# Kernel optimization log

Hardware: AMD Instinct MI355X
Metric: run time of the kernel (lower is better)

The kernel has to match this reference:

```python
import jax, jax.numpy as jnp
from jax import lax
import numpy as np

B, L, FEAT, EXTRA, K1 = 128, 128, 36, 12, 3
EMB, H, A, T_OUT = 6, 1024, 256, 24
CONV_OUT = FEAT - 2 * (K1 - 1)  # 32


def _conv1d(x, w):
    return lax.conv_general_dilated(x, w, (1,), 'VALID', dimension_numbers=('NCW', 'OIW', 'NCW'))


def _lstm(x_t, h, c, Wih, Whh, b):
    g = x_t @ Wih.T + h @ Whh.T + b
    i, f, gg, o = jnp.split(g, 4, axis=-1)
    c = jax.nn.sigmoid(f) * c + jax.nn.sigmoid(i) * jnp.tanh(gg)
    h = jax.nn.sigmoid(o) * jnp.tanh(c)
    return h, c


def setup_inputs():
    key = jax.random.key(0)
    ks = jax.random.split(key, 20)
    s = 0.05
    r = lambda k, sh: jax.random.normal(k, sh, jnp.float32) * s
    return {
        'x': jax.random.normal(ks[0], (B, L, FEAT + EXTRA), jnp.float32),
        'conv1_w': r(ks[1], (L, L, K1)), 'conv1_b': r(ks[2], (L,)),
        'conv2_w': r(ks[3], (L, L, K1)), 'conv2_b': r(ks[4], (L,)),
        'lin3_w': r(ks[5], (EMB, CONV_OUT)), 'lin3_b': r(ks[6], (EMB,)),
        'enc_Wih': r(ks[7], (4 * H, EMB + EXTRA)), 'enc_Whh': r(ks[8], (4 * H, H)), 'enc_b': r(ks[9], (4 * H,)),
        'attn_Wq': r(ks[10], (A, H)), 'attn_Wk': r(ks[11], (A, H)), 'attn_Wv': r(ks[12], (1, A)),
        'dec_Wih': r(ks[13], (4 * H, 2 * H)), 'dec_Whh': r(ks[14], (4 * H, H)), 'dec_b': r(ks[15], (4 * H,)),
        'out_w': r(ks[16], (1, H)), 'out_b': r(ks[17], (1,)),
    }


def reference(x, conv1_w, conv1_b, conv2_w, conv2_b, lin3_w, lin3_b,
              enc_Wih, enc_Whh, enc_b, attn_Wq, attn_Wk, attn_Wv,
              dec_Wih, dec_Whh, dec_b, out_w, out_b):
    # CNN feature extractor over the dense (short-interval) features
    dense = x[:, :, :FEAT]                                   # (B, L, 36)
    h1 = jax.nn.softplus(_conv1d(dense, conv1_w) + conv1_b[None, :, None])
    h2 = jax.nn.relu(_conv1d(h1, conv2_w) + conv2_b[None, :, None])  # (B, L, 32)
    lin = jnp.einsum('blf,ef->ble', h2, lin3_w) + lin3_b     # (B, L, EMB)
    lstm_in = jnp.concatenate([lin, x[:, :, FEAT:]], axis=2)  # (B, L, EMB+EXTRA)

    # LSTM encoder
    def enc_step(carry, xt):
        h, c = carry
        h, c = _lstm(xt, h, c, enc_Wih, enc_Whh, enc_b)
        return (h, c), h
    z = jnp.zeros((B, H), jnp.float32)
    (h, c), outs = lax.scan(enc_step, (z, z), lstm_in.transpose(1, 0, 2))
    enc_out = outs.transpose(1, 0, 2)                        # (B, L, H)
    s = enc_out[:, -1]

    # fixed-size key buffer; original appends s_t each step (lengths 128..151)
    M = L - 1 + T_OUT
    buf0 = jnp.zeros((B, M, H), jnp.float32).at[:, :L - 1].set(enc_out[:, :-1])
    pos = jnp.arange(M)

    def dec_step(carry, t):
        h, c, s, buf = carry
        buf = lax.dynamic_update_slice(buf, s[:, None, :], (0, L - 1 + t, 0))
        mask = (pos <= L - 1 + t).astype(buf.dtype)
        q = jnp.stack([h, c], axis=1)                        # (B, 2, H)
        qp = q @ attn_Wq.T                                   # (B, 2, A)
        kp = buf @ attn_Wk.T                                 # (B, M, A)
        feats = jnp.tanh(qp[:, :, None, :] + kp[:, None, :, :])  # (B, 2, M, A)
        scores = jnp.einsum('bnma,a->bnm', feats, attn_Wv[0])
        # original: softmax over dim=1 (query axis); mask keys post-softmax
        w = jax.nn.softmax(scores, axis=1) * mask[None, None, :]
        ctx = jnp.einsum('bnm,bmh->bnh', w, buf).reshape(B, 2 * H)
        h, c = _lstm(ctx, h, c, dec_Wih, dec_Whh, dec_b)
        y = (h @ out_w.T + out_b)[:, 0]
        return (h, c, h, buf), y

    _, ys = lax.scan(dec_step, (h, c, s, buf0), jnp.arange(T_OUT))
    return ys.T                                              # (B, T_OUT)
```

## Files before the change

### kernel.cpp

```cpp
#include <hip/hip_runtime.h>
#include <math.h>


#define NB 128
#define NL 128
#define NH 1024
#define NA 256
#define NT 24
#define NM 151

typedef __attribute__((ext_vector_type(8))) short bf16x8;
typedef __attribute__((ext_vector_type(8))) short s16x8;
typedef __attribute__((ext_vector_type(4))) float f32x4;

#define MFMA(a, b, acc) __builtin_amdgcn_mfma_f32_16x16x32_bf16(a, b, acc, 0, 0, 0)

#define I16_SCALE 32767.0f
#define I16_INV   (1.0f / 32767.0f)

__device__ __forceinline__ float sig_f(float x) {
  return 1.0f / (1.0f + __expf(-x));
}
__device__ __forceinline__ float tanh_f(float x) {
  x = fminf(9.0f, fmaxf(-9.0f, x));
  float e = __expf(2.0f * x);
  return (e - 1.0f) / (e + 1.0f);
}
__device__ __forceinline__ unsigned short f2bf(float f) {
  unsigned int u = __float_as_uint(f);
  u = (u + 0x7FFFu + ((u >> 16) & 1u)) >> 16;
  return (unsigned short)u;
}
__device__ __forceinline__ float bf2f(unsigned short u) {
  return __uint_as_float(((unsigned int)u) << 16);
}
__device__ __forceinline__ short f2i16(float f) {
  return (short)__float2int_rn(f * I16_SCALE);
}

__global__ __launch_bounds__(128) void conv_front(
    const float* __restrict__ x,
    const float* __restrict__ w1, const float* __restrict__ b1,
    const float* __restrict__ w2, const float* __restrict__ b2,
    const float* __restrict__ w3, const float* __restrict__ b3,
    float* __restrict__ lstm_in)
{
  int b = blockIdx.x;
  int t = threadIdx.x;
  __shared__ float d[128][36];
  __shared__ float h1[128][34];
  __shared__ float h2[128][32];

  const float* xr = x + (size_t)(b * NL + t) * 48;
  #pragma unroll
  for (int f = 0; f < 36; ++f) d[t][f] = xr[f];
  __syncthreads();

  float acc[34];
  {
    float bias = b1[t];
    #pragma unroll
    for (int w = 0; w < 34; ++w) acc[w] = bias;
  }
  const float* wr = w1 + t * 384;
  for (int ci = 0; ci < 128; ++ci) {
    float row[36];
    #pragma unroll
    for (int f = 0; f < 36; ++f) row[f] = d[ci][f];
    float wa = wr[ci * 3 + 0], wb = wr[ci * 3 + 1], wc = wr[ci * 3 + 2];
    #pragma unroll
    for (int w = 0; w < 34; ++w)
      acc[w] += row[w] * wa + row[w + 1] * wb + row[w + 2] * wc;
  }
  #pragma unroll
  for (int w = 0; w < 34; ++w) {
    float z = acc[w];
    h1[t][w] = (z > 20.0f) ? z : log1pf(__expf(z));
  }
  __syncthreads();

  float acc2[32];
  {
    float bias = b2[t];
    #pragma unroll
    for (int w = 0; w < 32; ++w) acc2[w] = bias;
  }
  const float* wr2 = w2 + t * 384;
  for (int ci = 0; ci < 128; ++ci) {
    float row[34];
    #pragma unroll
    for (int f = 0; f < 34; ++f) row[f] = h1[ci][f];
    float wa = wr2[ci * 3 + 0], wb = wr2[ci * 3 + 1], wc = wr2[ci * 3 + 2];
    #pragma unroll
    for (int w = 0; w < 32; ++w)
      acc2[w] += row[w] * wa + row[w + 1] * wb + row[w + 2] * wc;
  }
  #pragma unroll
  for (int w = 0; w < 32; ++w) h2[t][w] = fmaxf(acc2[w], 0.0f);
  __syncthreads();

  float* outr = lstm_in + (size_t)(b * NL + t) * 18;
  #pragma unroll
  for (int e = 0; e < 6; ++e) {
    float s = b3[e];
    #pragma unroll
    for (int f = 0; f < 32; ++f) s += h2[t][f] * w3[e * 32 + f];
    outr[e] = s;
  }
  #pragma unroll
  for (int j = 0; j < 12; ++j) outr[6 + j] = xr[36 + j];
}

__global__ void frag_w(const float* __restrict__ src, int K, int kshift,
                       unsigned short* __restrict__ hi,
                       unsigned short* __restrict__ lo, int ngroups)
{
  int o = blockIdx.x * 256 + threadIdx.x;
  if (o >= ngroups) return;
  int lane = o & 63;
  int ki = (o >> 6) & ((1 << kshift) - 1);
  int tile = (o >> (6 + kshift)) & 1;
  int bx = o >> (7 + kshift);
  int l15 = lane & 15, q = lane >> 4;
  int idx = tile * 16 + l15;
  int grow = (idx >> 3) * 1024 + bx * 8 + (idx & 7);
  const float* s = src + (size_t)grow * K + ki * 32 + q * 8;
  unsigned short hv[8], lv[8];
  #pragma unroll
  for (int j = 0; j < 8; ++j) {
    float v = s[j];
    hv[j] = f2bf(v);
    lv[j] = f2bf(v - bf2f(hv[j]));
  }
  size_t e = (size_t)o * 8;
  *(ushort4*)(hi + e) = make_ushort4(hv[0], hv[1], hv[2], hv[3]);
  *(ushort4*)(hi + e + 4) = make_ushort4(hv[4], hv[5], hv[6], hv[7]);
  *(ushort4*)(lo + e) = make_ushort4(lv[0], lv[1], lv[2], lv[3]);
  *(ushort4*)(lo + e + 4) = make_ushort4(lv[4], lv[5], lv[6], lv[7]);
}

__global__ void frag_wqk(const float* __restrict__ wq,
                         const float* __restrict__ wk,
                         unsigned short* __restrict__ hi,
                         unsigned short* __restrict__ lo)
{
  int o = blockIdx.x * 256 + threadIdx.x;
  if (o >= 65536) return;
  int lane = o & 63;
  int ki = (o >> 6) & 31;
  int ntile = o >> 11;
  int l15 = lane & 15, q = lane >> 4;
  int row = ntile * 16 + l15;
  int k = ki * 32 + q * 8;
  const float* s = (row < 256) ? (wq + (size_t)row * 1024 + k)
                               : (wk + (size_t)(row - 256) * 1024 + k);
  unsigned short hv[8], lv[8];
  #pragma unroll
  for (int j = 0; j < 8; ++j) {
    float v = s[j];
    hv[j] = f2bf(v);
    lv[j] = f2bf(v - bf2f(hv[j]));
  }
  size_t e = (size_t)o * 8;
  *(ushort4*)(hi + e) = make_ushort4(hv[0], hv[1], hv[2], hv[3]);
  *(ushort4*)(hi + e + 4) = make_ushort4(hv[4], hv[5], hv[6], hv[7]);
  *(ushort4*)(lo + e) = make_ushort4(lv[0], lv[1], lv[2], lv[3]);
  *(ushort4*)(lo + e + 4) = make_ushort4(lv[4], lv[5], lv[6], lv[7]);
}

__global__ void frag_wx(const float* __restrict__ wih,
                        unsigned short* __restrict__ hi,
                        unsigned short* __restrict__ lo)
{
  int o = blockIdx.x * 256 + threadIdx.x;
  if (o >= 16384) return;
  int lane = o & 63;
  int tile = (o >> 6) & 1;
  int bx = o >> 7;
  int l15 = lane & 15, q = lane >> 4;
  int idx = tile * 16 + l15;
  int grow = (idx >> 3) * 1024 + bx * 8 + (idx & 7);
  unsigned short hv[8], lv[8];
  #pragma unroll
  for (int j = 0; j < 8; ++j) {
    int k = q * 8 + j;
    float v = (k < 18) ? wih[(size_t)grow * 18 + k] : 0.0f;
    hv[j] = f2bf(v);
    lv[j] = f2bf(v - bf2f(hv[j]));
  }
  size_t e = (size_t)o * 8;
  *(ushort4*)(hi + e) = make_ushort4(hv[0], hv[1], hv[2], hv[3]);
  *(ushort4*)(hi + e + 4) = make_ushort4(hv[4], hv[5], hv[6], hv[7]);
  *(ushort4*)(lo + e) = make_ushort4(lv[0], lv[1], lv[2], lv[3]);
  *(ushort4*)(lo + e + 4) = make_ushort4(lv[4], lv[5], lv[6], lv[7]);
}

__global__ void frag_xs(const float* __restrict__ lstm_in,
                        unsigned short* __restrict__ hi,
                        unsigned short* __restrict__ lo)
{
  int o = blockIdx.x * 256 + threadIdx.x;
  if (o >= 65536) return;
  int lane = o & 63;
  int btile = (o >> 6) & 7;
  int t = o >> 9;
  int l15 = lane & 15, q = lane >> 4;
  int b = btile * 16 + l15;
  unsigned short hv[8], lv[8];
  #pragma unroll
  for (int j = 0; j < 8; ++j) {
    int k = q * 8 + j;
    float v = (k < 18) ? lstm_in[(size_t)(b * NL + t) * 18 + k] : 0.0f;
    hv[j] = f2bf(v);
    lv[j] = f2bf(v - bf2f(hv[j]));
  }
  size_t e = (size_t)o * 8;
  *(ushort4*)(hi + e) = make_ushort4(hv[0], hv[1], hv[2], hv[3]);
  *(ushort4*)(hi + e + 4) = make_ushort4(hv[4], hv[5], hv[6], hv[7]);
  *(ushort4*)(lo + e) = make_ushort4(lv[0], lv[1], lv[2], lv[3]);
  *(ushort4*)(lo + e + 4) = make_ushort4(lv[4], lv[5], lv[6], lv[7]);
}

__global__ void init_all(float* __restrict__ c,
                         unsigned short* __restrict__ hhi0,
                         unsigned short* __restrict__ hlo0,
                         float* __restrict__ out) {
  int i = blockIdx.x * 256 + threadIdx.x;
  if (i < NB * NH) { c[i] = 0.0f; hhi0[i] = 0; hlo0[i] = 0; }
  if (i < NB * NT) out[i] = 0.0f;
}

__global__ __launch_bounds__(512) void enc_step(
    const unsigned short* __restrict__ hfi_hi,
    const unsigned short* __restrict__ hfi_lo,
    unsigned short* __restrict__ hfo_hi,
    unsigned short* __restrict__ hfo_lo,
    const unsigned short* __restrict__ Wf_hi,
    const unsigned short* __restrict__ Wf_lo,
    const unsigned short* __restrict__ Wxf_hi,
    const unsigned short* __restrict__ Wxf_lo,
    const unsigned short* __restrict__ xsf_hi,
    const unsigned short* __restrict__ xsf_lo,
    const float* __restrict__ encb,
    float* __restrict__ c,
    short* __restrict__ buf,
    int t)
{
  __shared__ float G[2][128][33];
  int tid = threadIdx.x;
  int w8 = tid >> 6, lane = tid & 63;
  int grp = w8 >> 2, wm = w8 & 3;
  int l15 = lane & 15, q4 = (lane >> 4) * 4;
  int bx = blockIdx.x;
  int c0 = bx * 8;

  const unsigned short* B0h = Wf_hi + (size_t)(bx * 2 + 0) * 16384 + lane * 8;
  const unsigned short* B1h = Wf_hi + (size_t)(bx * 2 + 1) * 16384 + lane * 8;
  const unsigned short* B0l = Wf_lo + (size_t)(bx * 2 + 0) * 16384 + lane * 8;
  const unsigned short* B1l = Wf_lo + (size_t)(bx * 2 + 1) * 16384 + lane * 8;
  const unsigned short* A0h = hfi_hi + (size_t)(2 * wm) * 512 + lane * 8;
  const unsigned short* A1h = hfi_hi + (size_t)(2 * wm + 1) * 512 + lane * 8;
  const unsigned short* A0l = hfi_lo + (size_t)(2 * wm) * 512 + lane * 8;
  const unsigned short* A1l = hfi_lo + (size_t)(2 * wm + 1) * 512 + lane * 8;

  f32x4 a00 = {0,0,0,0}, a01 = {0,0,0,0}, a10 = {0,0,0,0}, a11 = {0,0,0,0};
  for (int i = 0; i < 16; ++i) {
    int ki = grp * 16 + i;
    size_t ao = (size_t)ki * 4096;
    size_t bo = (size_t)ki * 512;
    bf16x8 x0h = *(const bf16x8*)(A0h + ao);
    bf16x8 x0l = *(const bf16x8*)(A0l + ao);
    bf16x8 x1h = *(const bf16x8*)(A1h + ao);
    bf16x8 x1l = *(const bf16x8*)(A1l + ao);
    bf16x8 y0h = *(const bf16x8*)(B0h + bo);
    bf16x8 y0l = *(const bf16x8*)(B0l + bo);
    bf16x8 y1h = *(const bf16x8*)(B1h + bo);
    bf16x8 y1l = *(const bf16x8*)(B1l + bo);
    a00 = MFMA(x0h, y0h, a00); a00 = MFMA(x0l, y0h, a00); a00 = MFMA(x0h, y0l, a00);
    a01 = MFMA(x0h, y1h, a01); a01 = MFMA(x0l, y1h, a01); a01 = MFMA(x0h, y1l, a01);
    a10 = MFMA(x1h, y0h, a10); a10 = MFMA(x1l, y0h, a10); a10 = MFMA(x1h, y0l, a10);
    a11 = MFMA(x1h, y1h, a11); a11 = MFMA(x1l, y1h, a11); a11 = MFMA(x1h, y1l, a11);
  }
  if (grp == 0) {
    size_t xo0 = ((size_t)t * 8 + 2 * wm) * 512 + lane * 8;
    size_t xo1 = xo0 + 512;
    bf16x8 x0h = *(const bf16x8*)(xsf_hi + xo0);
    bf16x8 x0l = *(const bf16x8*)(xsf_lo + xo0);
    bf16x8 x1h = *(const bf16x8*)(xsf_hi + xo1);
    bf16x8 x1l = *(const bf16x8*)(xsf_lo + xo1);
    size_t wo0 = (size_t)(bx * 2 + 0) * 512 + lane * 8;
    size_t wo1 = (size_t)(bx * 2 + 1) * 512 + lane * 8;
    bf16x8 y0h = *(const bf16x8*)(Wxf_hi + wo0);
    bf16x8 y0l = *(const bf16x8*)(Wxf_lo + wo0);
    bf16x8 y1h = *(const bf16x8*)(Wxf_hi + wo1);
    bf16x8 y1l = *(const bf16x8*)(Wxf_lo + wo1);
    a00 = MFMA(x0h, y0h, a00); a00 = MFMA(x0l, y0h, a00); a00 = MFMA(x0h, y0l, a00);
    a01 = MFMA(x0h, y1h, a01); a01 = MFMA(x0l, y1h, a01); a01 = MFMA(x0h, y1l, a01);
    a10 = MFMA(x1h, y0h, a10); a10 = MFMA(x1l, y0h, a10); a10 = MFMA(x1h, y0l, a10);
    a11 = MFMA(x1h, y1h, a11); a11 = MFMA(x1l, y1h, a11); a11 = MFMA(x1h, y1l, a11);
  }
  #pragma unroll
  for (int r = 0; r < 4; ++r) {
    G[grp][32 * wm + q4 + r][l15]           = a00[r];
    G[grp][32 * wm + q4 + r][16 + l15]      = a01[r];
    G[grp][32 * wm + 16 + q4 + r][l15]      = a10[r];
    G[grp][32 * wm + 16 + q4 + r][16 + l15] = a11[r];
  }
  __syncthreads();

  if (tid < 256) {
    int b = tid >> 1;
    int kc = c0 + (tid & 1) * 4;
    int cc0 = (tid & 1) * 4;
    float4 cold = *(const float4*)(c + (size_t)b * NH + kc);
    float rc[4], rh[4];
    #pragma unroll
    for (int j = 0; j < 4; ++j) {
      int cc = cc0 + j;
      float gate[4];
      #pragma unroll
      for (int q = 0; q < 4; ++q) {
        int gi = q * 8 + cc;
        gate[q] = G[0][b][gi] + G[1][b][gi] + encb[q * NH + kc + j];
      }
      float co = (&cold.x)[j];
      float cn = sig_f(gate[1]) * co + sig_f(gate[0]) * tanh_f(gate[2]);
      float hn = sig_f(gate[3]) * tanh_f(cn);
      rc[j] = cn; rh[j] = hn;
    }
    *(float4*)(c + (size_t)b * NH + kc) = make_float4(rc[0], rc[1], rc[2], rc[3]);
    unsigned short hh[4], hl[4];
    short hq[4];
    #pragma unroll
    for (int j = 0; j < 4; ++j) {
      hh[j] = f2bf(rh[j]);
      hl[j] = f2bf(rh[j] - bf2f(hh[j]));
      hq[j] = f2i16(rh[j]);
    }
    int ki = kc >> 5, qq = (kc >> 3) & 3, j8 = kc & 7;
    size_t fo = (size_t)ki * 4096 + (b >> 4) * 512 + ((b & 15) + 16 * qq) * 8 + j8;
    *(ushort4*)(hfo_hi + fo) = make_ushort4(hh[0], hh[1], hh[2], hh[3]);
    *(ushort4*)(hfo_lo + fo) = make_ushort4(hl[0], hl[1], hl[2], hl[3]);
    *(short4*)(buf + (size_t)(b * NM + t) * NH + kc) =
        make_short4(hq[0], hq[1], hq[2], hq[3]);
  }
}

__global__ __launch_bounds__(256) void dec_prep(
    const unsigned short* __restrict__ hf_hi,
    const unsigned short* __restrict__ hf_lo,
    const float* __restrict__ c,
    unsigned short* __restrict__ qhi, unsigned short* __restrict__ qlo)
{
  int b = blockIdx.x;
  int j4 = threadIdx.x * 4;
  int ki = j4 >> 5, qq = (j4 >> 3) & 3, j8 = j4 & 7;
  size_t fh = (size_t)ki * 4096 + (b >> 4) * 512 + ((b & 15) + 16 * qq) * 8 + j8;
  ushort4 hv = *(const ushort4*)(hf_hi + fh);
  ushort4 lv = *(const ushort4*)(hf_lo + fh);
  float4 cv = *(const float4*)(c + (size_t)b * NH + j4);
  unsigned short ch[4], cl[4];
  float cf[4] = {cv.x, cv.y, cv.z, cv.w};
  #pragma unroll
  for (int k = 0; k < 4; ++k) {
    ch[k] = f2bf(cf[k]); cl[k] = f2bf(cf[k] - bf2f(ch[k]));
  }
  int rt = (2 * b) >> 4;
  int rl = ((2 * b) & 15) + 16 * qq;
  size_t fq = (size_t)ki * 8192 + rt * 512 + rl * 8 + j8;
  *(ushort4*)(qhi + fq) = hv;
  *(ushort4*)(qlo + fq) = lv;
  *(ushort4*)(qhi + fq + 8) = make_ushort4(ch[0], ch[1], ch[2], ch[3]);
  *(ushort4*)(qlo + fq + 8) = make_ushort4(cl[0], cl[1], cl[2], cl[3]);
}

__global__ __launch_bounds__(256) void gemm_qk(
    const unsigned short* __restrict__ Ahi, const unsigned short* __restrict__ Alo,
    const unsigned short* __restrict__ Bhi, const unsigned short* __restrict__ Blo,
    float* __restrict__ C)
{
  int tid = threadIdx.x;
  int w = tid >> 6, lane = tid & 63;
  int l15 = lane & 15, q4 = (lane >> 4) * 4;
  int mtile = blockIdx.x * 2 + (w >> 1);
  int ntile = blockIdx.y * 2 + (w & 1);

  const unsigned short* Ah = Ahi + (size_t)mtile * 512 + lane * 8;
  const unsigned short* Al = Alo + (size_t)mtile * 512 + lane * 8;
  const unsigned short* Bh = Bhi + (size_t)ntile * 16384 + lane * 8;
  const unsigned short* Bl = Blo + (size_t)ntile * 16384 + lane * 8;
  f32x4 acc = {0, 0, 0, 0};
  for (int ki = 0; ki < 32; ++ki) {
    size_t ao = (size_t)ki * 8192;
    size_t bo = (size_t)ki * 512;
    bf16x8 ah = *(const bf16x8*)(Ah + ao);
    bf16x8 al = *(const bf16x8*)(Al + ao);
    bf16x8 bh = *(const bf16x8*)(Bh + bo);
    bf16x8 bl = *(const bf16x8*)(Bl + bo);
    acc = MFMA(ah, bh, acc);
    acc = MFMA(al, bh, acc);
    acc = MFMA(ah, bl, acc);
  }
  #pragma unroll
  for (int r = 0; r < 4; ++r)
    C[(size_t)(mtile * 16 + q4 + r) * 512 + ntile * 16 + l15] = acc[r];
}

__global__ __launch_bounds__(256) void gemm_kp(
    const short* __restrict__ A,
    const unsigned short* __restrict__ Bhi,
    const unsigned short* __restrict__ Blo,
    unsigned short* __restrict__ C)
{
  int tid = threadIdx.x;
  int w = tid >> 6, lane = tid & 63;
  int l15 = lane & 15, q8 = (lane >> 4) * 8, q4 = (lane >> 4) * 4;
  size_t m0 = (size_t)blockIdx.x * 64;
  int n0 = blockIdx.y * 64 + w * 16;
  int ntile = 16 + blockIdx.y * 4 + w;

  const unsigned short* Bh = Bhi + (size_t)ntile * 16384 + lane * 8;
  const unsigned short* Bl = Blo + (size_t)ntile * 16384 + lane * 8;
  f32x4 acc[4] = {{0,0,0,0},{0,0,0,0},{0,0,0,0},{0,0,0,0}};
  for (int ki = 0; ki < 32; ++ki) {
    int ko = ki * 32 + q8;
    size_t bo = (size_t)ki * 512;
    bf16x8 bh = *(const bf16x8*)(Bh + bo);
    bf16x8 bl = *(const bf16x8*)(Bl + bo);
    #pragma unroll
    for (int i = 0; i < 4; ++i) {
      s16x8 av = *(const s16x8*)(A + (m0 + 16 * i + l15) * (size_t)NH + ko);
      bf16x8 ah;
      #pragma unroll
      for (int k = 0; k < 8; ++k)
        ah[k] = (short)f2bf((float)av[k] * I16_INV);
      acc[i] = MFMA(ah, bh, acc[i]);
      acc[i] = MFMA(ah, bl, acc[i]);
    }
  }
  #pragma unroll
  for (int i = 0; i < 4; ++i)
    #pragma unroll
    for (int r = 0; r < 4; ++r)
      C[(m0 + 16 * i + q4 + r) * NA + n0 + l15] = f2bf(acc[i][r]);
}

__global__ __launch_bounds__(256) void attn_kernel(
    const float* __restrict__ qkout,
    unsigned short* __restrict__ kp,
    const short* __restrict__ buf,
    const float* __restrict__ Wv,
    unsigned short* __restrict__ Xfhi,
    unsigned short* __restrict__ Xflo,
    int t)
{
  int b = blockIdx.x;
  int tid = threadIdx.x;
  int Mt = NL + t;
  __shared__ float sWv[256], q0[256], q1[256], kNew[256];
  __shared__ float sc[2][NM + 1];
  __shared__ float w0s[NM + 1], w1s[NM + 1];
  sWv[tid] = Wv[tid];
  q0[tid] = qkout[(size_t)(2 * b) * 512 + tid];
  q1[tid] = qkout[(size_t)(2 * b + 1) * 512 + tid];
  float kn = qkout[(size_t)(2 * b) * 512 + 256 + tid];
  kNew[tid] = kn;
  kp[((size_t)(b * NM) + (NL - 1 + t)) * NA + tid] = f2bf(kn);
  __syncthreads();

  for (int idx = tid; idx < 2 * Mt; idx += 256) {
    int m = idx >> 1, n = idx & 1;
    const float* q = n ? q1 : q0;
    float s = 0.0f;
    if (m == Mt - 1) {
      for (int a = 0; a < NA; ++a) s += tanh_f(q[a] + kNew[a]) * sWv[a];
    } else {
      const unsigned short* kpr = kp + ((size_t)(b * NM) + m) * NA;
      for (int a = 0; a < NA; a += 4) {
        ushort4 kv = *(const ushort4*)(kpr + a);
        s += tanh_f(q[a + 0] + bf2f(kv.x)) * sWv[a + 0];
        s += tanh_f(q[a + 1] + bf2f(kv.y)) * sWv[a + 1];
        s += tanh_f(q[a + 2] + bf2f(kv.z)) * sWv[a + 2];
        s += tanh_f(q[a + 3] + bf2f(kv.w)) * sWv[a + 3];
      }
    }
    sc[n][m] = s;
  }
  __syncthreads();
  for (int m = tid; m < Mt; m += 256) {
    float s0 = sc[0][m], s1 = sc[1][m];
    float mx = fmaxf(s0, s1);
    float e0 = __expf(s0 - mx), e1 = __expf(s1 - mx);
    float inv = 1.0f / (e0 + e1);
    w0s[m] = e0 * inv;
    w1s[m] = e1 * inv;
  }
  __syncthreads();

  float4 a0 = {0, 0, 0, 0}, a1 = {0, 0, 0, 0};
  const short* bb = buf + ((size_t)b * NM) * NH + tid * 4;
  for (int m = 0; m < Mt; ++m) {
    short4 v = *(const short4*)(bb + (size_t)m * NH);
    float vx = (float)v.x * I16_INV, vy = (float)v.y * I16_INV;
    float vz = (float)v.z * I16_INV, vw = (float)v.w * I16_INV;
    float w0 = w0s[m], w1 = w1s[m];
    a0.x += vx * w0; a0.y += vy * w0; a0.z += vz * w0; a0.w += vw * w0;
    a1.x += vx * w1; a1.y += vy * w1; a1.z += vz * w1; a1.w += vw * w1;
  }
  float v0[4] = {a0.x, a0.y, a0.z, a0.w};
  float v1[4] = {a1.x, a1.y, a1.z, a1.w};
  unsigned short h0[4], l0[4], h1v[4], l1v[4];
  #pragma unroll
  for (int k = 0; k < 4; ++k) {
    h0[k] = f2bf(v0[k]); l0[k] = f2bf(v0[k] - bf2f(h0[k]));
    h1v[k] = f2bf(v1[k]); l1v[k] = f2bf(v1[k] - bf2f(h1v[k]));
  }
  int k0 = tid * 4;
  size_t fo0 = (size_t)(k0 >> 5) * 4096 + (b >> 4) * 512 +
               ((b & 15) + 16 * ((k0 >> 3) & 3)) * 8 + (k0 & 7);
  int k1 = 1024 + tid * 4;
  size_t fo1 = (size_t)(k1 >> 5) * 4096 + (b >> 4) * 512 +
               ((b & 15) + 16 * ((k1 >> 3) & 3)) * 8 + (k1 & 7);
  *(ushort4*)(Xfhi + fo0) = make_ushort4(h0[0], h0[1], h0[2], h0[3]);
  *(ushort4*)(Xflo + fo0) = make_ushort4(l0[0], l0[1], l0[2], l0[3]);
  *(ushort4*)(Xfhi + fo1) = make_ushort4(h1v[0], h1v[1], h1v[2], h1v[3]);
  *(ushort4*)(Xflo + fo1) = make_ushort4(l1v[0], l1v[1], l1v[2], l1v[3]);
}

__global__ __launch_bounds__(512) void dec_step(
    const unsigned short* __restrict__ Xfhi,
    const unsigned short* __restrict__ Xflo,
    const unsigned short* __restrict__ qin_hi,
    const unsigned short* __restrict__ qin_lo,
    unsigned short* __restrict__ qout_hi,
    unsigned short* __restrict__ qout_lo,
    const unsigned short* __restrict__ Wdxf_hi,
    const unsigned short* __restrict__ Wdxf_lo,
    const unsigned short* __restrict__ Wdhf_hi,
    const unsigned short* __restrict__ Wdhf_lo,
    const float* __restrict__ decb,
    float* __restrict__ c,
    short* __restrict__ buf,
    const float* __restrict__ out_w, const float* __restrict__ out_b,
    float* __restrict__ out, int t)
{
  __shared__ float G[2][128][33];
  int tid = threadIdx.x;
  int w8 = tid >> 6, lane = tid & 63;
  int grp = w8 >> 2, wm = w8 & 3;
  int l15 = lane & 15, q4 = (lane >> 4) * 4;
  int bx = blockIdx.x;
  int c0 = bx * 8;

  f32x4 a00 = {0,0,0,0}, a01 = {0,0,0,0}, a10 = {0,0,0,0}, a11 = {0,0,0,0};

  {
    const unsigned short* W0h = Wdxf_hi + (size_t)(bx * 2 + 0) * 32768 + lane * 8;
    const unsigned short* W1h = Wdxf_hi + (size_t)(bx * 2 + 1) * 32768 + lane * 8;
    const unsigned short* W0l = Wdxf_lo + (size_t)(bx * 2 + 0) * 32768 + lane * 8;
    const unsigned short* W1l = Wdxf_lo + (size_t)(bx * 2 + 1) * 32768 + lane * 8;
    const unsigned short* X0h = Xfhi + (size_t)(2 * wm) * 512 + lane * 8;
    const unsigned short* X1h = Xfhi + (size_t)(2 * wm + 1) * 512 + lane * 8;
    const unsigned short* X0l = Xflo + (size_t)(2 * wm) * 512 + lane * 8;
    const unsigned short* X1l = Xflo + (size_t)(2 * wm + 1) * 512 + lane * 8;
    int klo = grp ? 48 : 0;
    int khi = grp ? 64 : 48;
    for (int ki = klo; ki < khi; ++ki) {
      size_t ao = (size_t)ki * 4096;
      size_t bo = (size_t)ki * 512;
      bf16x8 x0h = *(const bf16x8*)(X0h + ao);
      bf16x8 x0l = *(const bf16x8*)(X0l + ao);
      bf16x8 x1h = *(const bf16x8*)(X1h + ao);
      bf16x8 x1l = *(const bf16x8*)(X1l + ao);
      bf16x8 y0h = *(const bf16x8*)(W0h + bo);
      bf16x8 y0l = *(const bf16x8*)(W0l + bo);
      bf16x8 y1h = *(const bf16x8*)(W1h + bo);
      bf16x8 y1l = *(const bf16x8*)(W1l + bo);
      a00 = MFMA(x0h, y0h, a00); a00 = MFMA(x0l, y0h, a00); a00 = MFMA(x0h, y0l, a00);
      a01 = MFMA(x0h, y1h, a01); a01 = MFMA(x0l, y1h, a01); a01 = MFMA(x0h, y1l, a01);
      a10 = MFMA(x1h, y0h, a10); a10 = MFMA(x1l, y0h, a10); a10 = MFMA(x1h, y0l, a10);
      a11 = MFMA(x1h, y1h, a11); a11 = MFMA(x1l, y1h, a11); a11 = MFMA(x1h, y1l, a11);
    }
  }
  if (grp) {
    int qt0 = 4 * wm + (l15 >> 3);
    int ln = 2 * (l15 & 7) + 16 * (lane >> 4);
    const unsigned short* A0h = qin_hi + (size_t)qt0 * 512 + ln * 8;
    const unsigned short* A0l = qin_lo + (size_t)qt0 * 512 + ln * 8;
    const unsigned short* A1h = qin_hi + (size_t)(qt0 + 2) * 512 + ln * 8;
    const unsigned short* A1l = qin_lo + (size_t)(qt0 + 2) * 512 + ln * 8;
    const unsigned short* B0h = Wdhf_hi + (size_t)(bx * 2 + 0) * 16384 + lane * 8;
    const unsigned short* B1h = Wdhf_hi + (size_t)(bx * 2 + 1) * 16384 + lane * 8;
    const unsigned short* B0l = Wdhf_lo + (size_t)(bx * 2 + 0) * 16384 + lane * 8;
    const unsigned short* B1l = Wdhf_lo + (size_t)(bx * 2 + 1) * 16384 + lane * 8;
    for (int ki = 0; ki < 32; ++ki) {
      size_t ao = (size_t)ki * 8192;
      size_t bo = (size_t)ki * 512;
      bf16x8 x0h = *(const bf16x8*)(A0h + ao);
      bf16x8 x0l = *(const bf16x8*)(A0l + ao);
      bf16x8 x1h = *(const bf16x8*)(A1h + ao);
      bf16x8 x1l = *(const bf16x8*)(A1l + ao);
      bf16x8 y0h = *(const bf16x8*)(B0h + bo);
      bf16x8 y0l = *(const bf16x8*)(B0l + bo);
      bf16x8 y1h = *(const bf16x8*)(B1h + bo);
      bf16x8 y1l = *(const bf16x8*)(B1l + bo);
      a00 = MFMA(x0h, y0h, a00); a00 = MFMA(x0l, y0h, a00); a00 = MFMA(x0h, y0l, a00);
      a01 = MFMA(x0h, y1h, a01); a01 = MFMA(x0l, y1h, a01); a01 = MFMA(x0h, y1l, a01);
      a10 = MFMA(x1h, y0h, a10); a10 = MFMA(x1l, y0h, a10); a10 = MFMA(x1h, y0l, a10);
      a11 = MFMA(x1h, y1h, a11); a11 = MFMA(x1l, y1h, a11); a11 = MFMA(x1h, y1l, a11);
    }
  }
  #pragma unroll
  for (int r = 0; r < 4; ++r) {
    G[grp][32 * wm + q4 + r][l15]           = a00[r];
    G[grp][32 * wm + q4 + r][16 + l15]      = a01[r];
    G[grp][32 * wm + 16 + q4 + r][l15]      = a10[r];
    G[grp][32 * wm + 16 + q4 + r][16 + l15] = a11[r];
  }
  __syncthreads();

  if (tid < 256) {
    int b = tid >> 1;
    int kc = c0 + (tid & 1) * 4;
    int cc0 = (tid & 1) * 4;
    float4 cold = *(const float4*)(c + (size_t)b * NH + kc);
    float rc[4], rh[4];
    #pragma unroll
    for (int j = 0; j < 4; ++j) {
      int cc = cc0 + j;
      float gate[4];
      #pragma unroll
      for (int q = 0; q < 4; ++q) {
        int gi = q * 8 + cc;
        gate[q] = G[0][b][gi] + G[1][b][gi] + decb[q * NH + kc + j];
      }
      float co = (&cold.x)[j];
      float cn = sig_f(gate[1]) * co + sig_f(gate[0]) * tanh_f(gate[2]);
      float hn = sig_f(gate[3]) * tanh_f(cn);
      rc[j] = cn; rh[j] = hn;
    }
    *(float4*)(c + (size_t)b * NH + kc) = make_float4(rc[0], rc[1], rc[2], rc[3]);

    float py = 0.0f;
    #pragma unroll
    for (int j = 0; j < 4; ++j) py += rh[j] * out_w[kc + j];
    if (blockIdx.x == 0 && (tid & 1) == 0) py += out_b[0];
    py += __shfl_down(py, 1);
    if ((tid & 1) == 0) atomicAdd(&out[b * NT + t], py);

    if (t < NT - 1) {
      unsigned short hh[4], hl[4], ch[4], cl[4];
      short hq[4];
      #pragma unroll
      for (int j = 0; j < 4; ++j) {
        hh[j] = f2bf(rh[j]); hl[j] = f2bf(rh[j] - bf2f(hh[j]));
        ch[j] = f2bf(rc[j]); cl[j] = f2bf(rc[j] - bf2f(ch[j]));
        hq[j] = f2i16(rh[j]);
      }
      *(short4*)(buf + (size_t)(b * NM + NL + t) * NH + kc) =
          make_short4(hq[0], hq[1], hq[2], hq[3]);
      int ki = kc >> 5, qq = (kc >> 3) & 3, j8 = kc & 7;
      int rt = (2 * b) >> 4;
      int rl = ((2 * b) & 15) + 16 * qq;
      size_t fq = (size_t)ki * 8192 + rt * 512 + rl * 8 + j8;
      *(ushort4*)(qout_hi + fq) = make_ushort4(hh[0], hh[1], hh[2], hh[3]);
      *(ushort4*)(qout_lo + fq) = make_ushort4(hl[0], hl[1], hl[2], hl[3]);
      *(ushort4*)(qout_hi + fq + 8) = make_ushort4(ch[0], ch[1], ch[2], ch[3]);
      *(ushort4*)(qout_lo + fq + 8) = make_ushort4(cl[0], cl[1], cl[2], cl[3]);
    }
  }
}

extern "C" void kernel_launch(void* const* d_in, const int* in_sizes, int n_in,
                              void* d_out, int out_size, void* d_ws, size_t ws_size,
                              hipStream_t stream) {
  const float* x       = (const float*)d_in[0];
  const float* conv1_w = (const float*)d_in[1];
  const float* conv1_b = (const float*)d_in[2];
  const float* conv2_w = (const float*)d_in[3];
  const float* conv2_b = (const float*)d_in[4];
  const float* lin3_w  = (const float*)d_in[5];
  const float* lin3_b  = (const float*)d_in[6];
  const float* enc_Wih = (const float*)d_in[7];
  const float* enc_Whh = (const float*)d_in[8];
  const float* enc_b   = (const float*)d_in[9];
  const float* attn_Wq = (const float*)d_in[10];
  const float* attn_Wk = (const float*)d_in[11];
  const float* attn_Wv = (const float*)d_in[12];
  const float* dec_Wih = (const float*)d_in[13];
  const float* dec_Whh = (const float*)d_in[14];
  const float* dec_b   = (const float*)d_in[15];
  const float* out_w   = (const float*)d_in[16];
  const float* out_b   = (const float*)d_in[17];
  float* out = (float*)d_out;

  unsigned short* W = (unsigned short*)d_ws;
  short*          buf    = (short*)W;
  unsigned short* kp     = W + (size_t)19791872;
  unsigned short* qA_hi  = kp + 4947968;
  unsigned short* qA_lo  = qA_hi + 262144;
  unsigned short* qB_hi  = qA_lo + 262144;
  unsigned short* qB_lo  = qB_hi + 262144;
  unsigned short* Xf_hi  = qB_lo + 262144;
  unsigned short* Xf_lo  = Xf_hi + 262144;
  unsigned short* Wqkf_hi = Xf_lo + 262144;
  unsigned short* Wqkf_lo = Wqkf_hi + 524288;
  unsigned short* Wdhf_hi = Wqkf_lo + 524288;
  unsigned short* Wdhf_lo = Wdhf_hi + 4194304;
  unsigned short* Wdxf_hi = Wdhf_lo + 4194304;
  unsigned short* Wdxf_lo = Wdxf_hi + 8388608;
  float* c     = (float*)(Wdxf_lo + 8388608);
  float* qkout = c + 131072;
  unsigned short* hfA_hi = Wdxf_hi;
  unsigned short* hfA_lo = Wdxf_hi + 131072;
  unsigned short* hfB_hi = Wdxf_hi + 262144;
  unsigned short* hfB_lo = Wdxf_hi + 393216;
  unsigned short* xsf_hi = Wdxf_hi + 524288;
  unsigned short* xsf_lo = xsf_hi + 524288;
  unsigned short* Wxf_hi = xsf_lo + 524288;
  unsigned short* Wxf_lo = Wxf_hi + 131072;
  float* lstm_in = (float*)Wdxf_lo;

  init_all<<<512, 256, 0, stream>>>(c, hfA_hi, hfA_lo, out);
  conv_front<<<NB, 128, 0, stream>>>(x, conv1_w, conv1_b, conv2_w, conv2_b,
                                     lin3_w, lin3_b, lstm_in);
  frag_xs<<<256, 256, 0, stream>>>(lstm_in, xsf_hi, xsf_lo);
  frag_wx<<<64, 256, 0, stream>>>(enc_Wih, Wxf_hi, Wxf_lo);
  frag_w<<<2048, 256, 0, stream>>>(enc_Whh, 1024, 5, Wdhf_hi, Wdhf_lo, 524288);
  frag_wqk<<<256, 256, 0, stream>>>(attn_Wq, attn_Wk, Wqkf_hi, Wqkf_lo);

  for (int t = 0; t < NL; ++t) {
    const unsigned short* ih = (t & 1) ? hfB_hi : hfA_hi;
    const unsigned short* il = (t & 1) ? hfB_lo : hfA_lo;
    unsigned short* oh = (t & 1) ? hfA_hi : hfB_hi;
    unsigned short* ol = (t & 1) ? hfA_lo : hfB_lo;
    enc_step<<<128, 512, 0, stream>>>(ih, il, oh, ol, Wdhf_hi, Wdhf_lo,
                                      Wxf_hi, Wxf_lo, xsf_hi, xsf_lo,
                                      enc_b, c, buf, t);
  }

  dec_prep<<<NB, 256, 0, stream>>>(hfA_hi, hfA_lo, c, qA_hi, qA_lo);
  gemm_kp<<<dim3(302, 4), 256, 0, stream>>>(buf, Wqkf_hi, Wqkf_lo, kp);

  frag_w<<<4096, 256, 0, stream>>>(dec_Wih, 2048, 6, Wdxf_hi, Wdxf_lo, 1048576);
  frag_w<<<2048, 256, 0, stream>>>(dec_Whh, 1024, 5, Wdhf_hi, Wdhf_lo, 524288);

  for (int t = 0; t < NT; ++t) {
    const unsigned short* qih = (t & 1) ? qB_hi : qA_hi;
    const unsigned short* qil = (t & 1) ? qB_lo : qA_lo;
    unsigned short* qoh = (t & 1) ? qA_hi : qB_hi;
    unsigned short* qol = (t & 1) ? qA_lo : qB_lo;
    gemm_qk<<<dim3(8, 16), 256, 0, stream>>>(qih, qil, Wqkf_hi, Wqkf_lo, qkout);
    attn_kernel<<<NB, 256, 0, stream>>>(qkout, kp, buf, attn_Wv, Xf_hi, Xf_lo, t);
    dec_step<<<128, 512, 0, stream>>>(Xf_hi, Xf_lo, qih, qil, qoh, qol,
                                      Wdxf_hi, Wdxf_lo, Wdhf_hi, Wdhf_lo,
                                      dec_b, c, buf, out_w, out_b, out, t);
  }
}
```

Baseline: 4.696 ms.

## Halve per-block hidden columns to launch 256 LSTM step blocks

The encoder and decoder step kernels now compute 4 hidden units (one 16-column gate tile) per block instead of 8, so the grid doubles from 128 to 256 blocks to cover more of the CUs. The weight fragment layout is reorganised to match, and the gate epilogue uses one thread per batch row. gemm_qk is likewise split into smaller 128-thread blocks with twice as many blocks. The cost is that each block reloads the full h input fragments, so total activation traffic per step doubles, and there are twice as many atomic adds to the output.

```diff
diff --git a/kernel.cpp b/kernel.cpp
--- a/kernel.cpp
+++ b/kernel.cpp
@@ -111,19 +111,17 @@
   for (int j = 0; j < 12; ++j) outr[6 + j] = xr[36 + j];
 }
 
-__global__ void frag_w(const float* __restrict__ src, int K, int kshift,
-                       unsigned short* __restrict__ hi,
-                       unsigned short* __restrict__ lo, int ngroups)
+__global__ void frag_w4(const float* __restrict__ src, int K, int kshift,
+                        unsigned short* __restrict__ hi,
+                        unsigned short* __restrict__ lo, int ngroups)
 {
   int o = blockIdx.x * 256 + threadIdx.x;
   if (o >= ngroups) return;
   int lane = o & 63;
   int ki = (o >> 6) & ((1 << kshift) - 1);
-  int tile = (o >> (6 + kshift)) & 1;
-  int bx = o >> (7 + kshift);
+  int t2 = o >> (6 + kshift);
   int l15 = lane & 15, q = lane >> 4;
-  int idx = tile * 16 + l15;
-  int grow = (idx >> 3) * 1024 + bx * 8 + (idx & 7);
+  int grow = (l15 >> 2) * 1024 + t2 * 4 + (l15 & 3);
   const float* s = src + (size_t)grow * K + ki * 32 + q * 8;
   unsigned short hv[8], lv[8];
   #pragma unroll
@@ -168,18 +166,16 @@
   *(ushort4*)(lo + e + 4) = make_ushort4(lv[4], lv[5], lv[6], lv[7]);
 }
 
-__global__ void frag_wx(const float* __restrict__ wih,
-                        unsigned short* __restrict__ hi,
-                        unsigned short* __restrict__ lo)
+__global__ void frag_wx4(const float* __restrict__ wih,
+                         unsigned short* __restrict__ hi,
+                         unsigned short* __restrict__ lo)
 {
   int o = blockIdx.x * 256 + threadIdx.x;
   if (o >= 16384) return;
   int lane = o & 63;
-  int tile = (o >> 6) & 1;
-  int bx = o >> 7;
+  int t2 = o >> 6;
   int l15 = lane & 15, q = lane >> 4;
-  int idx = tile * 16 + l15;
-  int grow = (idx >> 3) * 1024 + bx * 8 + (idx & 7);
+  int grow = (l15 >> 2) * 1024 + t2 * 4 + (l15 & 3);
   unsigned short hv[8], lv[8];
   #pragma unroll
   for (int j = 0; j < 8; ++j) {
@@ -246,24 +242,21 @@
     short* __restrict__ buf,
     int t)
 {
-  __shared__ float G[2][128][33];
+  __shared__ float G[2][128][17];
   int tid = threadIdx.x;
   int w8 = tid >> 6, lane = tid & 63;
   int grp = w8 >> 2, wm = w8 & 3;
   int l15 = lane & 15, q4 = (lane >> 4) * 4;
   int bx = blockIdx.x;
-  int c0 = bx * 8;
-
-  const unsigned short* B0h = Wf_hi + (size_t)(bx * 2 + 0) * 16384 + lane * 8;
-  const unsigned short* B1h = Wf_hi + (size_t)(bx * 2 + 1) * 16384 + lane * 8;
-  const unsigned short* B0l = Wf_lo + (size_t)(bx * 2 + 0) * 16384 + lane * 8;
-  const unsigned short* B1l = Wf_lo + (size_t)(bx * 2 + 1) * 16384 + lane * 8;
+
+  const unsigned short* Bh = Wf_hi + (size_t)bx * 16384 + lane * 8;
+  const unsigned short* Bl = Wf_lo + (size_t)bx * 16384 + lane * 8;
   const unsigned short* A0h = hfi_hi + (size_t)(2 * wm) * 512 + lane * 8;
   const unsigned short* A1h = hfi_hi + (size_t)(2 * wm + 1) * 512 + lane * 8;
   const unsigned short* A0l = hfi_lo + (size_t)(2 * wm) * 512 + lane * 8;
   const unsigned short* A1l = hfi_lo + (size_t)(2 * wm + 1) * 512 + lane * 8;
 
-  f32x4 a00 = {0,0,0,0}, a01 = {0,0,0,0}, a10 = {0,0,0,0}, a11 = {0,0,0,0};
+  f32x4 a00 = {0,0,0,0}, a10 = {0,0,0,0};
   for (int i = 0; i < 16; ++i) {
     int ki = grp * 16 + i;
     size_t ao = (size_t)ki * 4096;
@@ -272,14 +265,10 @@
     bf16x8 x0l = *(const bf16x8*)(A0l + ao);
     bf16x8 x1h = *(const bf16x8*)(A1h + ao);
     bf16x8 x1l = *(const bf16x8*)(A1l + ao);
-    bf16x8 y0h = *(const bf16x8*)(B0h + bo);
-    bf16x8 y0l = *(const bf16x8*)(B0l + bo);
-    bf16x8 y1h = *(const bf16x8*)(B1h + bo);
-    bf16x8 y1l = *(const bf16x8*)(B1l + bo);
-    a00 = MFMA(x0h, y0h, a00); a00 = MFMA(x0l, y0h, a00); a00 = MFMA(x0h, y0l, a00);
-    a01 = MFMA(x0h, y1h, a01); a01 = MFMA(x0l, y1h, a01); a01 = MFMA(x0h, y1l, a01);
-    a10 = MFMA(x1h, y0h, a10); a10 = MFMA(x1l, y0h, a10); a10 = MFMA(x1h, y0l, a10);
-    a11 = MFMA(x1h, y1h, a11); a11 = MFMA(x1l, y1h, a11); a11 = MFMA(x1h, y1l, a11);
+    bf16x8 yh = *(const bf16x8*)(Bh + bo);
+    bf16x8 yl = *(const bf16x8*)(Bl + bo);
+    a00 = MFMA(x0h, yh, a00); a00 = MFMA(x0l, yh, a00); a00 = MFMA(x0h, yl, a00);
+    a10 = MFMA(x1h, yh, a10); a10 = MFMA(x1l, yh, a10); a10 = MFMA(x1h, yl, a10);
   }
   if (grp == 0) {
     size_t xo0 = ((size_t)t * 8 + 2 * wm) * 512 + lane * 8;
@@ -288,39 +277,30 @@
     bf16x8 x0l = *(const bf16x8*)(xsf_lo + xo0);
     bf16x8 x1h = *(const bf16x8*)(xsf_hi + xo1);
     bf16x8 x1l = *(const bf16x8*)(xsf_lo + xo1);
-    size_t wo0 = (size_t)(bx * 2 + 0) * 512 + lane * 8;
-    size_t wo1 = (size_t)(bx * 2 + 1) * 512 + lane * 8;
-    bf16x8 y0h = *(const bf16x8*)(Wxf_hi + wo0);
-    bf16x8 y0l = *(const bf16x8*)(Wxf_lo + wo0);
-    bf16x8 y1h = *(const bf16x8*)(Wxf_hi + wo1);
-    bf16x8 y1l = *(const bf16x8*)(Wxf_lo + wo1);
-    a00 = MFMA(x0h, y0h, a00); a00 = MFMA(x0l, y0h, a00); a00 = MFMA(x0h, y0l, a00);
-    a01 = MFMA(x0h, y1h, a01); a01 = MFMA(x0l, y1h, a01); a01 = MFMA(x0h, y1l, a01);
-    a10 = MFMA(x1h, y0h, a10); a10 = MFMA(x1l, y0h, a10); a10 = MFMA(x1h, y0l, a10);
-    a11 = MFMA(x1h, y1h, a11); a11 = MFMA(x1l, y1h, a11); a11 = MFMA(x1h, y1l, a11);
+    size_t wo = (size_t)bx * 512 + lane * 8;
+    bf16x8 yh = *(const bf16x8*)(Wxf_hi + wo);
+    bf16x8 yl = *(const bf16x8*)(Wxf_lo + wo);
+    a00 = MFMA(x0h, yh, a00); a00 = MFMA(x0l, yh, a00); a00 = MFMA(x0h, yl, a00);
+    a10 = MFMA(x1h, yh, a10); a10 = MFMA(x1l, yh, a10); a10 = MFMA(x1h, yl, a10);
   }
   #pragma unroll
   for (int r = 0; r < 4; ++r) {
-    G[grp][32 * wm + q4 + r][l15]           = a00[r];
-    G[grp][32 * wm + q4 + r][16 + l15]      = a01[r];
-    G[grp][32 * wm + 16 + q4 + r][l15]      = a10[r];
-    G[grp][32 * wm + 16 + q4 + r][16 + l15] = a11[r];
+    G[grp][32 * wm + q4 + r][l15]      = a00[r];
+    G[grp][32 * wm + 16 + q4 + r][l15] = a10[r];
   }
   __syncthreads();
 
-  if (tid < 256) {
-    int b = tid >> 1;
-    int kc = c0 + (tid & 1) * 4;
-    int cc0 = (tid & 1) * 4;
+  if (tid < 128) {
+    int b = tid;
+    int kc = bx * 4;
     float4 cold = *(const float4*)(c + (size_t)b * NH + kc);
     float rc[4], rh[4];
     #pragma unroll
     for (int j = 0; j < 4; ++j) {
-      int cc = cc0 + j;
       float gate[4];
       #pragma unroll
       for (int q = 0; q < 4; ++q) {
-        int gi = q * 8 + cc;
+        int gi = q * 4 + j;
         gate[q] = G[0][b][gi] + G[1][b][gi] + encb[q * NH + kc + j];
       }
       float co = (&cold.x)[j];
@@ -374,7 +354,7 @@
   *(ushort4*)(qlo + fq + 8) = make_ushort4(cl[0], cl[1], cl[2], cl[3]);
 }
 
-__global__ __launch_bounds__(256) void gemm_qk(
+__global__ __launch_bounds__(128) void gemm_qk(
     const unsigned short* __restrict__ Ahi, const unsigned short* __restrict__ Alo,
     const unsigned short* __restrict__ Bhi, const unsigned short* __restrict__ Blo,
     float* __restrict__ C)
@@ -382,8 +362,8 @@
   int tid = threadIdx.x;
   int w = tid >> 6, lane = tid & 63;
   int l15 = lane & 15, q4 = (lane >> 4) * 4;
-  int mtile = blockIdx.x * 2 + (w >> 1);
-  int ntile = blockIdx.y * 2 + (w & 1);
+  int mtile = blockIdx.x;
+  int ntile = blockIdx.y * 2 + w;
 
   const unsigned short* Ah = Ahi + (size_t)mtile * 512 + lane * 8;
   const unsigned short* Al = Alo + (size_t)mtile * 512 + lane * 8;
@@ -544,21 +524,18 @@
     const float* __restrict__ out_w, const float* __restrict__ out_b,
     float* __restrict__ out, int t)
 {
-  __shared__ float G[2][128][33];
+  __shared__ float G[2][128][17];
   int tid = threadIdx.x;
   int w8 = tid >> 6, lane = tid & 63;
   int grp = w8 >> 2, wm = w8 & 3;
   int l15 = lane & 15, q4 = (lane >> 4) * 4;
   int bx = blockIdx.x;
-  int c0 = bx * 8;
-
-  f32x4 a00 = {0,0,0,0}, a01 = {0,0,0,0}, a10 = {0,0,0,0}, a11 = {0,0,0,0};
+
+  f32x4 a00 = {0,0,0,0}, a10 = {0,0,0,0};
 
   {
-    const unsigned short* W0h = Wdxf_hi + (size_t)(bx * 2 + 0) * 32768 + lane * 8;
-    const unsigned short* W1h = Wdxf_hi + (size_t)(bx * 2 + 1) * 32768 + lane * 8;
-    const unsigned short* W0l = Wdxf_lo + (size_t)(bx * 2 + 0) * 32768 + lane * 8;
-    const unsigned short* W1l = Wdxf_lo + (size_t)(bx * 2 + 1) * 32768 + lane * 8;
+    const unsigned short* Wh = Wdxf_hi + (size_t)bx * 32768 + lane * 8;
+    const unsigned short* Wl = Wdxf_lo + (size_t)bx * 32768 + lane * 8;
     const unsigned short* X0h = Xfhi + (size_t)(2 * wm) * 512 + lane * 8;
     const unsigned short* X1h = Xfhi + (size_t)(2 * wm + 1) * 512 + lane * 8;
     const unsigned short* X0l = Xflo + (size_t)(2 * wm) * 512 + lane * 8;
@@ -572,14 +549,10 @@
       bf16x8 x0l = *(const bf16x8*)(X0l + ao);
       bf16x8 x1h = *(const bf16x8*)(X1h + ao);
       bf16x8 x1l = *(const bf16x8*)(X1l + ao);
-      bf16x8 y0h = *(const bf16x8*)(W0h + bo);
-      bf16x8 y0l = *(const bf16x8*)(W0l + bo);
-      bf16x8 y1h = *(const bf16x8*)(W1h + bo);
-      bf16x8 y1l = *(const bf16x8*)(W1l + bo);
-      a00 = MFMA(x0h, y0h, a00); a00 = MFMA(x0l, y0h, a00); a00 = MFMA(x0h, y0l, a00);
-      a01 = MFMA(x0h, y1h, a01); a01 = MFMA(x0l, y1h, a01); a01 = MFMA(x0h, y1l, a01);
-      a10 = MFMA(x1h, y0h, a10); a10 = MFMA(x1l, y0h, a10); a10 = MFMA(x1h, y0l, a10);
-      a11 = MFMA(x1h, y1h, a11); a11 = MFMA(x1l, y1h, a11); a11 = MFMA(x1h, y1l, a11);
+      bf16x8 yh = *(const bf16x8*)(Wh + bo);
+      bf16x8 yl = *(const bf16x8*)(Wl + bo);
+      a00 = MFMA(x0h, yh, a00); a00 = MFMA(x0l, yh, a00); a00 = MFMA(x0h, yl, a00);
+      a10 = MFMA(x1h, yh, a10); a10 = MFMA(x1l, yh, a10); a10 = MFMA(x1h, yl, a10);
     }
   }
   if (grp) {
@@ -589,10 +562,8 @@
     const unsigned short* A0l = qin_lo + (size_t)qt0 * 512 + ln * 8;
     const unsigned short* A1h = qin_hi + (size_t)(qt0 + 2) * 512 + ln * 8;
     const unsigned short* A1l = qin_lo + (size_t)(qt0 + 2) * 512 + ln * 8;
-    const unsigned short* B0h = Wdhf_hi + (size_t)(bx * 2 + 0) * 16384 + lane * 8;
-    const unsigned short* B1h = Wdhf_hi + (size_t)(bx * 2 + 1) * 16384 + lane * 8;
-    const unsigned short* B0l = Wdhf_lo + (size_t)(bx * 2 + 0) * 16384 + lane * 8;
-    const unsigned short* B1l = Wdhf_lo + (size_t)(bx * 2 + 1) * 16384 + lane * 8;
+    const unsigned short* Bh = Wdhf_hi + (size_t)bx * 16384 + lane * 8;
+    const unsigned short* Bl = Wdhf_lo + (size_t)bx * 16384 + lane * 8;
     for (int ki = 0; ki < 32; ++ki) {
       size_t ao = (size_t)ki * 8192;
       size_t bo = (size_t)ki * 512;
@@ -600,38 +571,30 @@
       bf16x8 x0l = *(const bf16x8*)(A0l + ao);
       bf16x8 x1h = *(const bf16x8*)(A1h + ao);
       bf16x8 x1l = *(const bf16x8*)(A1l + ao);
-      bf16x8 y0h = *(const bf16x8*)(B0h + bo);
-      bf16x8 y0l = *(const bf16x8*)(B0l + bo);
-      bf16x8 y1h = *(const bf16x8*)(B1h + bo);
-      bf16x8 y1l = *(const bf16x8*)(B1l + bo);
-      a00 = MFMA(x0h, y0h, a00); a00 = MFMA(x0l, y0h, a00); a00 = MFMA(x0h, y0l, a00);
-      a01 = MFMA(x0h, y1h, a01); a01 = MFMA(x0l, y1h, a01); a01 = MFMA(x0h, y1l, a01);
-      a10 = MFMA(x1h, y0h, a10); a10 = MFMA(x1l, y0h, a10); a10 = MFMA(x1h, y0l, a10);
-      a11 = MFMA(x1h, y1h, a11); a11 = MFMA(x1l, y1h, a11); a11 = MFMA(x1h, y1l, a11);
+      bf16x8 yh = *(const bf16x8*)(Bh + bo);
+      bf16x8 yl = *(const bf16x8*)(Bl + bo);
+      a00 = MFMA(x0h, yh, a00); a00 = MFMA(x0l, yh, a00); a00 = MFMA(x0h, yl, a00);
+      a10 = MFMA(x1h, yh, a10); a10 = MFMA(x1l, yh, a10); a10 = MFMA(x1h, yl, a10);
     }
   }
   #pragma unroll
   for (int r = 0; r < 4; ++r) {
-    G[grp][32 * wm + q4 + r][l15]           = a00[r];
-    G[grp][32 * wm + q4 + r][16 + l15]      = a01[r];
-    G[grp][32 * wm + 16 + q4 + r][l15]      = a10[r];
-    G[grp][32 * wm + 16 + q4 + r][16 + l15] = a11[r];
+    G[grp][32 * wm + q4 + r][l15]      = a00[r];
+    G[grp][32 * wm + 16 + q4 + r][l15] = a10[r];
   }
   __syncthreads();
 
-  if (tid < 256) {
-    int b = tid >> 1;
-    int kc = c0 + (tid & 1) * 4;
-    int cc0 = (tid & 1) * 4;
+  if (tid < 128) {
+    int b = tid;
+    int kc = bx * 4;
     float4 cold = *(const float4*)(c + (size_t)b * NH + kc);
     float rc[4], rh[4];
     #pragma unroll
     for (int j = 0; j < 4; ++j) {
-      int cc = cc0 + j;
       float gate[4];
       #pragma unroll
       for (int q = 0; q < 4; ++q) {
-        int gi = q * 8 + cc;
+        int gi = q * 4 + j;
         gate[q] = G[0][b][gi] + G[1][b][gi] + decb[q * NH + kc + j];
       }
       float co = (&cold.x)[j];
@@ -644,9 +607,8 @@
     float py = 0.0f;
     #pragma unroll
     for (int j = 0; j < 4; ++j) py += rh[j] * out_w[kc + j];
-    if (blockIdx.x == 0 && (tid & 1) == 0) py += out_b[0];
-    py += __shfl_down(py, 1);
-    if ((tid & 1) == 0) atomicAdd(&out[b * NT + t], py);
+    if (bx == 0) py += out_b[0];
+    atomicAdd(&out[b * NT + t], py);
 
     if (t < NT - 1) {
       unsigned short hh[4], hl[4], ch[4], cl[4];
@@ -725,8 +687,8 @@
   conv_front<<<NB, 128, 0, stream>>>(x, conv1_w, conv1_b, conv2_w, conv2_b,
                                      lin3_w, lin3_b, lstm_in);
   frag_xs<<<256, 256, 0, stream>>>(lstm_in, xsf_hi, xsf_lo);
-  frag_wx<<<64, 256, 0, stream>>>(enc_Wih, Wxf_hi, Wxf_lo);
-  frag_w<<<2048, 256, 0, stream>>>(enc_Whh, 1024, 5, Wdhf_hi, Wdhf_lo, 524288);
+  frag_wx4<<<64, 256, 0, stream>>>(enc_Wih, Wxf_hi, Wxf_lo);
+  frag_w4<<<2048, 256, 0, stream>>>(enc_Whh, 1024, 5, Wdhf_hi, Wdhf_lo, 524288);
   frag_wqk<<<256, 256, 0, stream>>>(attn_Wq, attn_Wk, Wqkf_hi, Wqkf_lo);
 
   for (int t = 0; t < NL; ++t) {
@@ -734,7 +696,7 @@
     const unsigned short* il = (t & 1) ? hfB_lo : hfA_lo;
     unsigned short* oh = (t & 1) ? hfA_hi : hfB_hi;
     unsigned short* ol = (t & 1) ? hfA_lo : hfB_lo;
-    enc_step<<<128, 512, 0, stream>>>(ih, il, oh, ol, Wdhf_hi, Wdhf_lo,
+    enc_step<<<256, 512, 0, stream>>>(ih, il, oh, ol, Wdhf_hi, Wdhf_lo,
                                       Wxf_hi, Wxf_lo, xsf_hi, xsf_lo,
                                       enc_b, c, buf, t);
   }
@@ -742,17 +704,17 @@
   dec_prep<<<NB, 256, 0, stream>>>(hfA_hi, hfA_lo, c, qA_hi, qA_lo);
   gemm_kp<<<dim3(302, 4), 256, 0, stream>>>(buf, Wqkf_hi, Wqkf_lo, kp);
 
-  frag_w<<<4096, 256, 0, stream>>>(dec_Wih, 2048, 6, Wdxf_hi, Wdxf_lo, 1048576);
-  frag_w<<<2048, 256, 0, stream>>>(dec_Whh, 1024, 5, Wdhf_hi, Wdhf_lo, 524288);
+  frag_w4<<<4096, 256, 0, stream>>>(dec_Wih, 2048, 6, Wdxf_hi, Wdxf_lo, 1048576);
+  frag_w4<<<2048, 256, 0, stream>>>(dec_Whh, 1024, 5, Wdhf_hi, Wdhf_lo, 524288);
 
   for (int t = 0; t < NT; ++t) {
     const unsigned short* qih = (t & 1) ? qB_hi : qA_hi;
     const unsigned short* qil = (t & 1) ? qB_lo : qA_lo;
     unsigned short* qoh = (t & 1) ? qA_hi : qB_hi;
     unsigned short* qol = (t & 1) ? qA_lo : qB_lo;
-    gemm_qk<<<dim3(8, 16), 256, 0, stream>>>(qih, qil, Wqkf_hi, Wqkf_lo, qkout);
+    gemm_qk<<<dim3(16, 16), 128, 0, stream>>>(qih, qil, Wqkf_hi, Wqkf_lo, qkout);
     attn_kernel<<<NB, 256, 0, stream>>>(qkout, kp, buf, attn_Wv, Xf_hi, Xf_lo, t);
-    dec_step<<<128, 512, 0, stream>>>(Xf_hi, Xf_lo, qih, qil, qoh, qol,
+    dec_step<<<256, 512, 0, stream>>>(Xf_hi, Xf_lo, qih, qil, qoh, qol,
                                       Wdxf_hi, Wdxf_lo, Wdhf_hi, Wdhf_lo,
                                       dec_b, c, buf, out_w, out_b, out, t);
   }
```

Result: no change. 4.622 ms (-1.6%).
